# Kernel optimization log

Measured on AMD Instinct MI355X. Metric: run time of the kernel, lower is better.

## Reference

```python
import jax, jax.numpy as jnp
import numpy as np

A = 1000          # nr_assets
LQ = 2048         # len_quote
C = 3             # channels == nr_in
H = 10            # sub_net_out (LSTM hidden)
NLAYER = 3        # hidden_l
HID = A * H       # 10000
MID = HID // 2    # 5000
NPOS = A + 1      # 1001
NOUT = 2001       # nr_out


def lstm_step0(x, w_ih, b_ih, b_hh):
    # One LSTM cell step from zero (h0, c0). w_hh @ h0 == 0 so w_hh drops out
    # of the forward math (it still exists as a parameter). torch gate order i,f,g,o.
    gates = x @ w_ih.T + b_ih + b_hh            # [A, 4H]
    i, f, g, o = jnp.split(gates, 4, axis=-1)
    c = jax.nn.sigmoid(i) * jnp.tanh(g)          # f*c0 == 0
    return jax.nn.sigmoid(o) * jnp.tanh(c)       # [A, H]


def setup_inputs() -> dict:
    key = jax.random.key(0)
    ks = jax.random.split(key, 20)
    s = 0.1
    inp = {
        "quotes": jax.random.normal(ks[0], (A, LQ, C), dtype=jnp.float32),
        "position": jax.random.normal(ks[1], (NPOS,), dtype=jnp.float32),
        # LSTM layer 0 (input C), layers 1,2 (input H)
        "w_ih_l0": s * jax.random.normal(ks[2], (4 * H, C), dtype=jnp.float32),
        "w_hh_l0": s * jax.random.normal(ks[3], (4 * H, H), dtype=jnp.float32),
        "b_ih_l0": s * jax.random.normal(ks[4], (4 * H,), dtype=jnp.float32),
        "b_hh_l0": s * jax.random.normal(ks[5], (4 * H,), dtype=jnp.float32),
        "w_ih_l1": s * jax.random.normal(ks[6], (4 * H, H), dtype=jnp.float32),
        "w_hh_l1": s * jax.random.normal(ks[7], (4 * H, H), dtype=jnp.float32),
        "b_ih_l1": s * jax.random.normal(ks[8], (4 * H,), dtype=jnp.float32),
        "b_hh_l1": s * jax.random.normal(ks[9], (4 * H,), dtype=jnp.float32),
        "w_ih_l2": s * jax.random.normal(ks[10], (4 * H, H), dtype=jnp.float32),
        "w_hh_l2": s * jax.random.normal(ks[11], (4 * H, H), dtype=jnp.float32),
        "b_ih_l2": s * jax.random.normal(ks[12], (4 * H,), dtype=jnp.float32),
        "b_hh_l2": s * jax.random.normal(ks[13], (4 * H,), dtype=jnp.float32),
        "w1": s * jax.random.normal(ks[14], (MID, HID), dtype=jnp.float32),
        "b1": s * jax.random.normal(ks[15], (MID,), dtype=jnp.float32),
        "w2": s * jax.random.normal(ks[16], (NOUT, MID + NPOS), dtype=jnp.float32),
        "b2": s * jax.random.normal(ks[17], (NOUT,), dtype=jnp.float32),
    }
    return inp


def reference(quotes, position,
              w_ih_l0, w_hh_l0, b_ih_l0, b_hh_l0,
              w_ih_l1, w_hh_l1, b_ih_l1, b_hh_l1,
              w_ih_l2, w_hh_l2, b_ih_l2, b_hh_l2,
              w1, b1, w2, b2):
    # Original loop: per-asset quote.view(1, len_quote, C) -> seq_len-1 LSTM with
    # batch=len_quote from zero state; out[:, -1] keeps only the last time row.
    # Equivalent batched form: one 3-layer LSTM cell step on quotes[:, -1, :].
    x = quotes[:, -1, :]                          # [A, C]
    h = lstm_step0(x, w_ih_l0, b_ih_l0, b_hh_l0)  # [A, H]
    h = lstm_step0(h, w_ih_l1, b_ih_l1, b_hh_l1)
    h = lstm_step0(h, w_ih_l2, b_ih_l2, b_hh_l2)
    h = jnp.tanh(h)
    conc = h.reshape(1, -1)                       # concat of [1,H] per asset == [1, A*H]
    lin = jnp.tanh(conc @ w1.T + b1)              # [1, MID]
    out_pos = jnp.concatenate([lin, position.reshape(1, -1)], axis=1)
    return out_pos @ w2.T + b2                    # [1, NOUT]
```

## Files before the change

### kernel.cpp

```cpp
#include <hip/hip_runtime.h>
#include <math.h>

#define A_N   1000
#define LQ_N  2048
#define C_N   3
#define H_N   10
#define HID_N 10000
#define MID_N 5000
#define NPOS_N 1001
#define NOUT_N 2001
#define W2COLS 6001

__device__ __forceinline__ float sigmoidf_(float x) { return 1.0f / (1.0f + expf(-x)); }

__global__ void __launch_bounds__(256) lstm_head(
    const float* __restrict__ quotes,
    const float* __restrict__ wih0, const float* __restrict__ bih0, const float* __restrict__ bhh0,
    const float* __restrict__ wih1, const float* __restrict__ bih1, const float* __restrict__ bhh1,
    const float* __restrict__ wih2, const float* __restrict__ bih2, const float* __restrict__ bhh2,
    float* __restrict__ conc)
{
    int a = blockIdx.x * blockDim.x + threadIdx.x;
    if (a >= A_N) return;

    const float* q = quotes + (size_t)a * LQ_N * C_N + (size_t)(LQ_N - 1) * C_N;
    float x0 = q[0], x1 = q[1], x2 = q[2];

    float g[40];
    float h[H_N];

    #pragma unroll
    for (int j = 0; j < 40; ++j)
        g[j] = x0 * wih0[j * 3 + 0] + x1 * wih0[j * 3 + 1] + x2 * wih0[j * 3 + 2]
             + bih0[j] + bhh0[j];
    #pragma unroll
    for (int k = 0; k < H_N; ++k) {
        float cc = sigmoidf_(g[k]) * tanhf(g[20 + k]);
        h[k] = sigmoidf_(g[30 + k]) * tanhf(cc);
    }

    #pragma unroll
    for (int j = 0; j < 40; ++j) {
        float s = bih1[j] + bhh1[j];
        #pragma unroll
        for (int k = 0; k < H_N; ++k) s += h[k] * wih1[j * 10 + k];
        g[j] = s;
    }
    float h2[H_N];
    #pragma unroll
    for (int k = 0; k < H_N; ++k) {
        float cc = sigmoidf_(g[k]) * tanhf(g[20 + k]);
        h2[k] = sigmoidf_(g[30 + k]) * tanhf(cc);
    }

    #pragma unroll
    for (int j = 0; j < 40; ++j) {
        float s = bih2[j] + bhh2[j];
        #pragma unroll
        for (int k = 0; k < H_N; ++k) s += h2[k] * wih2[j * 10 + k];
        g[j] = s;
    }
    #pragma unroll
    for (int k = 0; k < H_N; ++k) {
        float cc = sigmoidf_(g[k]) * tanhf(g[20 + k]);
        float hh = sigmoidf_(g[30 + k]) * tanhf(cc);
        conc[a * H_N + k] = tanhf(hh);
    }
}

__global__ void __launch_bounds__(256) mv1(
    const float* __restrict__ w1, const float* __restrict__ b1,
    const float* __restrict__ conc, float* __restrict__ lin)
{
    int gwave = (blockIdx.x * 256 + threadIdx.x) >> 6;
    int lane  = threadIdx.x & 63;
    if (gwave >= MID_N) return;

    const float4* row = reinterpret_cast<const float4*>(w1 + (size_t)gwave * HID_N);
    const float4* v   = reinterpret_cast<const float4*>(conc);

    float acc = 0.0f;
    const int n4 = HID_N / 4;
    for (int i = lane; i < n4; i += 64) {
        float4 a = row[i];
        float4 b = v[i];
        acc += a.x * b.x + a.y * b.y + a.z * b.z + a.w * b.w;
    }
    #pragma unroll
    for (int off = 32; off > 0; off >>= 1) acc += __shfl_down(acc, off, 64);
    if (lane == 0) lin[gwave] = tanhf(acc + b1[gwave]);
}

__global__ void __launch_bounds__(256) mv2(
    const float* __restrict__ w2, const float* __restrict__ b2,
    const float* __restrict__ lin, const float* __restrict__ pos,
    float* __restrict__ out)
{
    int row = blockIdx.x;
    const float* wr = w2 + (size_t)row * W2COLS;

    float acc = 0.0f;
    for (int j = threadIdx.x; j < W2COLS; j += 256) {
        float v = (j < MID_N) ? lin[j] : pos[j - MID_N];
        acc += wr[j] * v;
    }
    #pragma unroll
    for (int off = 32; off > 0; off >>= 1) acc += __shfl_down(acc, off, 64);

    __shared__ float red[4];
    int lane = threadIdx.x & 63;
    int wid  = threadIdx.x >> 6;
    if (lane == 0) red[wid] = acc;
    __syncthreads();
    if (threadIdx.x == 0)
        out[row] = red[0] + red[1] + red[2] + red[3] + b2[row];
}

extern "C" void kernel_launch(void* const* d_in, const int* in_sizes, int n_in,
                              void* d_out, int out_size, void* d_ws, size_t ws_size,
                              hipStream_t stream)
{
    const float* quotes = (const float*)d_in[0];
    const float* pos    = (const float*)d_in[1];
    const float* wih0   = (const float*)d_in[2];
    const float* bih0   = (const float*)d_in[4];
    const float* bhh0   = (const float*)d_in[5];
    const float* wih1   = (const float*)d_in[6];
    const float* bih1   = (const float*)d_in[8];
    const float* bhh1   = (const float*)d_in[9];
    const float* wih2   = (const float*)d_in[10];
    const float* bih2   = (const float*)d_in[12];
    const float* bhh2   = (const float*)d_in[13];
    const float* w1     = (const float*)d_in[14];
    const float* b1     = (const float*)d_in[15];
    const float* w2     = (const float*)d_in[16];
    const float* b2     = (const float*)d_in[17];
    float* out = (float*)d_out;

    float* conc = (float*)d_ws;
    float* lin  = conc + HID_N;

    lstm_head<<<(A_N + 255) / 256, 256, 0, stream>>>(
        quotes, wih0, bih0, bhh0, wih1, bih1, bhh1, wih2, bih2, bhh2, conc);

    mv1<<<MID_N / 4, 256, 0, stream>>>(w1, b1, conc, lin);

    mv2<<<NOUT_N, 256, 0, stream>>>(w2, b2, lin, pos, out);
}
```

Before: 64.63 us.

## Split w2 matvec, compute position part alongside mv1, vectorize and unroll loads

The position segment of the second matvec does not depend on the hidden layer, so it now runs in the same launch as the first matvec, and its result plus the bias goes to a workspace partial. The remaining second matvec uses one wave per row with float4 loads of w2, using a per-row alignment prologue and a tail. Both matvec loops are unrolled by two with separate accumulators to keep more loads in flight. This moves about a sixth of the w2 traffic off the critical path and drops the block-level shared-memory reduction, at the cost of a more complex alignment scheme and an extra workspace round-trip.

```diff
diff --git a/kernel.cpp b/kernel.cpp
--- a/kernel.cpp
+++ b/kernel.cpp
@@ -1,17 +1,27 @@
 #include <hip/hip_runtime.h>
 #include <math.h>
 
-#define A_N   1000
-#define LQ_N  2048
-#define C_N   3
-#define H_N   10
-#define HID_N 10000
-#define MID_N 5000
+#define A_N    1000
+#define LQ_N   2048
+#define C_N    3
+#define H_N    10
+#define HID_N  10000
+#define MID_N  5000
 #define NPOS_N 1001
 #define NOUT_N 2001
 #define W2COLS 6001
 
+#define MV1_BLOCKS (MID_N / 4)
+#define POS_BLOCKS ((NOUT_N + 3) / 4)
+#define B_GRID     (MV1_BLOCKS + POS_BLOCKS)
+
 __device__ __forceinline__ float sigmoidf_(float x) { return 1.0f / (1.0f + expf(-x)); }
+
+__device__ __forceinline__ float wave_reduce(float acc) {
+    #pragma unroll
+    for (int off = 32; off > 0; off >>= 1) acc += __shfl_down(acc, off, 64);
+    return acc;
+}
 
 __global__ void __launch_bounds__(256) lstm_head(
     const float* __restrict__ quotes,
@@ -68,52 +78,89 @@
     }
 }
 
-__global__ void __launch_bounds__(256) mv1(
+__global__ void __launch_bounds__(256) fused_mv1_pos(
     const float* __restrict__ w1, const float* __restrict__ b1,
-    const float* __restrict__ conc, float* __restrict__ lin)
+    const float* __restrict__ conc, float* __restrict__ lin,
+    const float* __restrict__ w2, const float* __restrict__ b2,
+    const float* __restrict__ pos, float* __restrict__ partial)
 {
-    int gwave = (blockIdx.x * 256 + threadIdx.x) >> 6;
-    int lane  = threadIdx.x & 63;
-    if (gwave >= MID_N) return;
+    int lane = threadIdx.x & 63;
+    int wid  = threadIdx.x >> 6;
 
-    const float4* row = reinterpret_cast<const float4*>(w1 + (size_t)gwave * HID_N);
-    const float4* v   = reinterpret_cast<const float4*>(conc);
+    if (blockIdx.x < MV1_BLOCKS) {
+        int row = blockIdx.x * 4 + wid;
+        const float4* rb = reinterpret_cast<const float4*>(w1 + (size_t)row * HID_N);
+        const float4* v  = reinterpret_cast<const float4*>(conc);
+        const int n4 = HID_N / 4;
+
+        float acc0 = 0.0f, acc1 = 0.0f;
+        int i = lane;
+        for (; i + 64 < n4; i += 128) {
+            float4 a0 = rb[i];      float4 c0 = v[i];
+            float4 a1 = rb[i + 64]; float4 c1 = v[i + 64];
+            acc0 += a0.x * c0.x + a0.y * c0.y + a0.z * c0.z + a0.w * c0.w;
+            acc1 += a1.x * c1.x + a1.y * c1.y + a1.z * c1.z + a1.w * c1.w;
+        }
+        if (i < n4) {
+            float4 a = rb[i]; float4 c = v[i];
+            acc0 += a.x * c.x + a.y * c.y + a.z * c.z + a.w * c.w;
+        }
+        float acc = wave_reduce(acc0 + acc1);
+        if (lane == 0) lin[row] = tanhf(acc + b1[row]);
+    } else {
+        int row = (blockIdx.x - MV1_BLOCKS) * 4 + wid;
+        if (row >= NOUT_N) return;
+        const float* wr = w2 + (size_t)row * W2COLS + MID_N;
+
+        float acc = 0.0f;
+        for (int j = lane; j < NPOS_N; j += 64)
+            acc += wr[j] * pos[j];
+        acc = wave_reduce(acc);
+        if (lane == 0) partial[row] = acc + b2[row];
+    }
+}
+
+__global__ void __launch_bounds__(256) mv2_main(
+    const float* __restrict__ w2, const float* __restrict__ lin,
+    const float* __restrict__ partial, float* __restrict__ out)
+{
+    int lane = threadIdx.x & 63;
+    int wid  = threadIdx.x >> 6;
+    int row  = blockIdx.x * 4 + wid;
+    if (row >= NOUT_N) return;
+
+    const float* wr = w2 + (size_t)row * W2COLS;
+    const int p = (4 - (row & 3)) & 3;
+    const int n    = MID_N - p;
+    const int n4   = n >> 2;
+    const int tail = n & 3;
 
     float acc = 0.0f;
-    const int n4 = HID_N / 4;
-    for (int i = lane; i < n4; i += 64) {
-        float4 a = row[i];
-        float4 b = v[i];
-        acc += a.x * b.x + a.y * b.y + a.z * b.z + a.w * b.w;
+    if (lane < p) acc += wr[lane] * lin[lane];
+
+    const float4* rb = reinterpret_cast<const float4*>(wr + p);
+    float acc1 = 0.0f;
+    int i = lane;
+    for (; i + 64 < n4; i += 128) {
+        float4 a0 = rb[i];
+        float4 a1 = rb[i + 64];
+        int j0 = p + 4 * i;
+        int j1 = p + 4 * (i + 64);
+        acc  += a0.x * lin[j0] + a0.y * lin[j0 + 1] + a0.z * lin[j0 + 2] + a0.w * lin[j0 + 3];
+        acc1 += a1.x * lin[j1] + a1.y * lin[j1 + 1] + a1.z * lin[j1 + 2] + a1.w * lin[j1 + 3];
     }
-    #pragma unroll
-    for (int off = 32; off > 0; off >>= 1) acc += __shfl_down(acc, off, 64);
-    if (lane == 0) lin[gwave] = tanhf(acc + b1[gwave]);
-}
+    if (i < n4) {
+        float4 a = rb[i];
+        int j = p + 4 * i;
+        acc += a.x * lin[j] + a.y * lin[j + 1] + a.z * lin[j + 2] + a.w * lin[j + 3];
+    }
+    if (lane < tail) {
+        int j = p + 4 * n4 + lane;
+        acc += wr[j] * lin[j];
+    }
 
-__global__ void __launch_bounds__(256) mv2(
-    const float* __restrict__ w2, const float* __restrict__ b2,
-    const float* __restrict__ lin, const float* __restrict__ pos,
-    float* __restrict__ out)
-{
-    int row = blockIdx.x;
-    const float* wr = w2 + (size_t)row * W2COLS;
-
-    float acc = 0.0f;
-    for (int j = threadIdx.x; j < W2COLS; j += 256) {
-        float v = (j < MID_N) ? lin[j] : pos[j - MID_N];
-        acc += wr[j] * v;
-    }
-    #pragma unroll
-    for (int off = 32; off > 0; off >>= 1) acc += __shfl_down(acc, off, 64);
-
-    __shared__ float red[4];
-    int lane = threadIdx.x & 63;
-    int wid  = threadIdx.x >> 6;
-    if (lane == 0) red[wid] = acc;
-    __syncthreads();
-    if (threadIdx.x == 0)
-        out[row] = red[0] + red[1] + red[2] + red[3] + b2[row];
+    float s = wave_reduce(acc + acc1);
+    if (lane == 0) out[row] = partial[row] + s;
 }
 
 extern "C" void kernel_launch(void* const* d_in, const int* in_sizes, int n_in,
@@ -137,13 +184,15 @@
     const float* b2     = (const float*)d_in[17];
     float* out = (float*)d_out;
 
-    float* conc = (float*)d_ws;
-    float* lin  = conc + HID_N;
+    float* conc    = (float*)d_ws;
+    float* lin     = conc + HID_N;
+    float* partial = lin + MID_N;
 
     lstm_head<<<(A_N + 255) / 256, 256, 0, stream>>>(
         quotes, wih0, bih0, bhh0, wih1, bih1, bhh1, wih2, bih2, bhh2, conc);
 
-    mv1<<<MID_N / 4, 256, 0, stream>>>(w1, b1, conc, lin);
+    fused_mv1_pos<<<B_GRID, 256, 0, stream>>>(
+        w1, b1, conc, lin, w2, b2, pos, partial);
 
-    mv2<<<NOUT_N, 256, 0, stream>>>(w2, b2, lin, pos, out);
+    mv2_main<<<POS_BLOCKS, 256, 0, stream>>>(w2, lin, partial, out);
 }
```

Result: slower. 69.09 us (+6.9%).
